# Optimization experiments

Measured on AMD Instinct MI355X. Metric: run time of the kernel, lower is better.

## Reference

```python
import jax, jax.numpy as jnp
import numpy as np

HIDDEN = 2048
HEAD_SIZE = 8
EXTRA = 4
NH = HEAD_SIZE * EXTRA          # 32 effective heads
D = HIDDEN // (HEAD_SIZE * 16)  # 16 per-head dim
PROJ = NH * D                   # 512
# NOTE: the torch module scales by att_size**-0.5 where att_size is the
# PRE-division value hidden//head_size//4 = 64, not the per-head dim D=16.
SCALE = (HIDDEN // HEAD_SIZE // EXTRA) ** -0.5


def _xavier(key, out_dim, in_dim):
    bound = float(np.sqrt(6.0 / (in_dim + out_dim)))
    return jax.random.uniform(key, (out_dim, in_dim), jnp.float32, -bound, bound)


def setup_inputs() -> dict:
    key = jax.random.key(0)
    ks = jax.random.split(key, 7)
    B, S = 2, 2048
    return {
        "q": jax.random.normal(ks[0], (B, S, HIDDEN), jnp.float32),
        "k": jax.random.normal(ks[1], (B, S, HIDDEN), jnp.float32),
        "v": jax.random.normal(ks[2], (B, S, HIDDEN), jnp.float32),
        "Wq": _xavier(ks[3], PROJ, HIDDEN),
        "Wk": _xavier(ks[4], PROJ, HIDDEN),
        "Wv": _xavier(ks[5], PROJ, HIDDEN),
        "Wo": _xavier(ks[6], HIDDEN, PROJ),
    }


def reference(q, k, v, Wq, Wk, Wv, Wo):
    B, S, _ = q.shape
    # projections (torch Linear: x @ W.T), reshape to [B,S,heads,d]
    qh = (q @ Wq.T).reshape(B, S, NH, D)
    kh = (k @ Wk.T).reshape(B, S, NH, D)
    vh = (v @ Wv.T).reshape(B, S, NH, D)
    scores = jnp.einsum("bshd,bthd->bhst", qh * SCALE, kh)  # [B,NH,S,S]
    attn = jax.nn.softmax(scores, axis=-1)
    out = jnp.einsum("bhst,bthd->bshd", attn, vh).reshape(B, S, PROJ)
    return out @ Wo.T  # [B,S,HIDDEN]
```

## Files before the change

### kernel.cpp

```cpp
#include <hip/hip_runtime.h>

#define HIDDEN 2048
#define NH 32
#define HD 16
#define PROJ 512
#define SEQ 2048

using f32x4    = __attribute__((ext_vector_type(4))) float;
using bf16x8   = __attribute__((ext_vector_type(8))) __bf16;

__device__ __forceinline__ unsigned short f2bf(float x) {
  unsigned int u = __float_as_uint(x);
  u += 0x7FFFu + ((u >> 16) & 1u);
  return (unsigned short)(u >> 16);
}

__device__ __forceinline__ f32x4 mfma_bf16(bf16x8 a, bf16x8 b, f32x4 c) {
  return __builtin_amdgcn_mfma_f32_16x16x32_bf16(a, b, c, 0, 0, 0);
}

#define GLDS16(gptr, lptr)                                              \
  __builtin_amdgcn_global_load_lds(                                     \
      (const __attribute__((address_space(1))) unsigned int*)(gptr),    \
      (__attribute__((address_space(3))) unsigned int*)(lptr), 16, 0, 0)

__global__ __launch_bounds__(256)
void convw_kernel(const float* __restrict__ Wq, const float* __restrict__ Wk,
                  const float* __restrict__ Wv, const float* __restrict__ Wo,
                  unsigned short* __restrict__ Wqb, unsigned short* __restrict__ Wkb,
                  unsigned short* __restrict__ Wvb, unsigned short* __restrict__ Wob) {
  const int z = blockIdx.y;
  const float* src = (z == 0) ? Wq : (z == 1) ? Wk : (z == 2) ? Wv : Wo;
  unsigned short* dst = (z == 0) ? Wqb : (z == 1) ? Wkb : (z == 2) ? Wvb : Wob;
  const size_t i = ((size_t)blockIdx.x * 256 + threadIdx.x) * 4;
  f32x4 v = *(const f32x4*)(src + i);
  uint2 p;
  p.x = f2bf(v[0]) | ((unsigned)f2bf(v[1]) << 16);
  p.y = f2bf(v[2]) | ((unsigned)f2bf(v[3]) << 16);
  *(uint2*)(dst + i) = p;
}

__global__ __launch_bounds__(256)
void convx_kernel(const float* __restrict__ q, const float* __restrict__ k,
                  const float* __restrict__ v,
                  unsigned short* __restrict__ qb, unsigned short* __restrict__ kb,
                  unsigned short* __restrict__ vb) {
  const int z = blockIdx.y;
  const float* src = (z == 0) ? q : (z == 1) ? k : v;
  unsigned short* dst = (z == 0) ? qb : (z == 1) ? kb : vb;
  const size_t i = ((size_t)blockIdx.x * 256 + threadIdx.x) * 4;
  f32x4 x = *(const f32x4*)(src + i);
  uint2 p;
  p.x = f2bf(x[0]) | ((unsigned)f2bf(x[1]) << 16);
  p.y = f2bf(x[2]) | ((unsigned)f2bf(x[3]) << 16);
  *(uint2*)(dst + i) = p;
}

__global__ __launch_bounds__(256)
void proj_kernel(const unsigned short* __restrict__ qb,
                 const unsigned short* __restrict__ kb,
                 const unsigned short* __restrict__ vb,
                 const unsigned short* __restrict__ Wqb,
                 const unsigned short* __restrict__ Wkb,
                 const unsigned short* __restrict__ Wvb,
                 unsigned short* __restrict__ qh, unsigned short* __restrict__ kh,
                 unsigned short* __restrict__ vt) {
  const int lin = blockIdx.x;
  const int e = lin & 7;
  const int t = lin >> 3;
  const int colt = t & 3;
  const int j = t >> 2;
  const int y = e + 8 * j;
  const int z = y >> 6;
  const int row0 = (y & 63) * 64;
  const int col0 = colt * 128;

  const unsigned short* A = (z == 0) ? qb : (z == 1) ? kb : vb;
  const unsigned short* Wb = (z == 0) ? Wqb : (z == 1) ? Wkb : Wvb;
  const float scale = (z == 0) ? 0.18033688011112042f  : 1.0f;

  __shared__ unsigned short As[64 * 32];
  __shared__ unsigned short Bs[128 * 32];

  const int tid = threadIdx.x;
  const int w = tid >> 6;
  const int lane = tid & 63;
  const int ln = lane & 15;
  const int qd = lane >> 4;
  const int wm = w >> 1, wn = w & 1;

  const int aM = tid >> 2;
  const int aG = (tid & 3) ^ (aM & 3);
  int bN[2], bG[2];
#pragma unroll
  for (int s = 0; s < 2; s++) {
    int L = s * 256 + tid;
    bN[s] = L >> 2;
    bG[s] = (L & 3) ^ (bN[s] & 3);
  }

  f32x4 acc[2][4];
#pragma unroll
  for (int mi = 0; mi < 2; mi++)
#pragma unroll
    for (int ni = 0; ni < 4; ni++) acc[mi][ni] = (f32x4){0.f, 0.f, 0.f, 0.f};

  for (int k0 = 0; k0 < HIDDEN; k0 += 32) {
    GLDS16(A + (size_t)(row0 + aM) * HIDDEN + k0 + aG * 8, &As[tid * 8]);
#pragma unroll
    for (int s = 0; s < 2; s++)
      GLDS16(Wb + (size_t)(col0 + bN[s]) * HIDDEN + k0 + bG[s] * 8,
             &Bs[(s * 256 + tid) * 8]);
    __syncthreads();

    bf16x8 af[2], bfv[4];
#pragma unroll
    for (int mi = 0; mi < 2; mi++) {
      int m = wm * 32 + mi * 16 + ln;
      af[mi] = *(const bf16x8*)&As[(m * 4 + (qd ^ (m & 3))) * 8];
    }
#pragma unroll
    for (int ni = 0; ni < 4; ni++) {
      int n = wn * 64 + ni * 16 + ln;
      bfv[ni] = *(const bf16x8*)&Bs[(n * 4 + (qd ^ (n & 3))) * 8];
    }
#pragma unroll
    for (int mi = 0; mi < 2; mi++)
#pragma unroll
      for (int ni = 0; ni < 4; ni++)
        acc[mi][ni] = mfma_bf16(af[mi], bfv[ni], acc[mi][ni]);
    __syncthreads();
  }

  if (z == 2) {
#pragma unroll
    for (int mi = 0; mi < 2; mi++)
#pragma unroll
      for (int ni = 0; ni < 4; ni++) {
        int h = (col0 + wn * 64 + ni * 16) >> 4;
        int grow0 = row0 + wm * 32 + mi * 16 + qd * 4;
        int b = grow0 >> 11, s0 = grow0 & 2047;
        uint2 o2;
        o2.x = f2bf(acc[mi][ni][0]) | ((unsigned)f2bf(acc[mi][ni][1]) << 16);
        o2.y = f2bf(acc[mi][ni][2]) | ((unsigned)f2bf(acc[mi][ni][3]) << 16);
        *(uint2*)&vt[((size_t)(b * NH + h) * HD + ln) * SEQ + s0] = o2;
      }
  } else {
    unsigned short* out = (z == 0) ? qh : kh;
#pragma unroll
    for (int mi = 0; mi < 2; mi++)
#pragma unroll
      for (int ni = 0; ni < 4; ni++) {
        int h = (col0 + wn * 64 + ni * 16) >> 4;
#pragma unroll
        for (int r = 0; r < 4; r++) {
          int grow = row0 + wm * 32 + mi * 16 + qd * 4 + r;
          int b = grow >> 11, s = grow & 2047;
          out[((size_t)(b * NH + h) * SEQ + s) * HD + ln] = f2bf(acc[mi][ni][r] * scale);
        }
      }
  }
}

__global__ __launch_bounds__(256, 4)
void flash_kernel(const unsigned short* __restrict__ qh,
                  const unsigned short* __restrict__ kh,
                  const unsigned short* __restrict__ vt,
                  unsigned short* __restrict__ attnb) {
  const int bh = blockIdx.x;
  const int b = bh >> 5, h = bh & 31;
  const int q0 = blockIdx.y * 128;
  const size_t hoff = (size_t)bh * SEQ * HD;
  const unsigned short* Qp = qh + hoff;
  const unsigned short* Kp = kh + hoff;
  const unsigned short* Vth = vt + hoff;

  __shared__ unsigned short Qs[128 * 16];
  __shared__ unsigned short Ks[2][128 * 16];
  __shared__ unsigned short Vts[2][256 * 8];
  __shared__ unsigned short Ps[4][32 * 40];
  __shared__ __align__(16) unsigned short Zz[8];

  const int tid = threadIdx.x;
  const int w = tid >> 6;
  const int lane = tid & 63;
  const int ln = lane & 15;
  const int qd = lane >> 4;
  const bool hiq = (qd >= 2);

  if (tid < 8) Zz[tid] = 0;

  const int vD = tid >> 4;
  const int vG = (tid & 15) ^ vD;

  GLDS16(Qp + (size_t)q0 * HD + tid * 8, &Qs[tid * 8]);
  GLDS16(Kp + tid * 8, &Ks[0][tid * 8]);
  GLDS16(Vth + (size_t)vD * SEQ + vG * 8, &Vts[0][tid * 8]);
  __syncthreads();

  bf16x8 aq[2];
#pragma unroll
  for (int ni = 0; ni < 2; ni++) {
    const unsigned short* src =
        hiq ? Zz : &Qs[(w * 32 + ni * 16 + ln) * 16 + (qd & 1) * 8];
    aq[ni] = *(const bf16x8*)src;
  }

  float lsum[2] = {0.f, 0.f};
  f32x4 o_acc[2] = {{0.f, 0.f, 0.f, 0.f}, {0.f, 0.f, 0.f, 0.f}};
  unsigned short* Pw = &Ps[w][0];

  for (int t = 0; t < 16; t++) {
    const int buf = t & 1;
    if (t < 15) {
      GLDS16(Kp + (size_t)(t + 1) * 2048 + tid * 8, &Ks[buf ^ 1][tid * 8]);
      GLDS16(Vth + (size_t)vD * SEQ + (t + 1) * 128 + vG * 8, &Vts[buf ^ 1][tid * 8]);
    }
    const unsigned short* Kb = &Ks[buf][0];
    const unsigned short* Vb = &Vts[buf][0];

#pragma unroll
    for (int c = 0; c < 4; c++) {
      f32x4 sc[2][2];
#pragma unroll
      for (int hf = 0; hf < 2; hf++) {
        int tile = c * 2 + hf;
        const unsigned short* asrc =
            hiq ? Zz : &Kb[(tile * 16 + ln) * 16 + (qd & 1) * 8];
        bf16x8 ak = *(const bf16x8*)asrc;
#pragma unroll
        for (int ni = 0; ni < 2; ni++)
          sc[ni][hf] = mfma_bf16(ak, aq[ni], (f32x4){0.f, 0.f, 0.f, 0.f});
      }
      bf16x8 av = *(const bf16x8*)&Vb[(ln * 16 + ((c * 4 + qd) ^ ln)) * 8];

#pragma unroll
      for (int ni = 0; ni < 2; ni++) {
        float e0 = __builtin_amdgcn_exp2f(sc[ni][0][0]);
        float e1 = __builtin_amdgcn_exp2f(sc[ni][0][1]);
        float e2 = __builtin_amdgcn_exp2f(sc[ni][0][2]);
        float e3 = __builtin_amdgcn_exp2f(sc[ni][0][3]);
        float e4 = __builtin_amdgcn_exp2f(sc[ni][1][0]);
        float e5 = __builtin_amdgcn_exp2f(sc[ni][1][1]);
        float e6 = __builtin_amdgcn_exp2f(sc[ni][1][2]);
        float e7 = __builtin_amdgcn_exp2f(sc[ni][1][3]);
        lsum[ni] += ((e0 + e1) + (e2 + e3)) + ((e4 + e5) + (e6 + e7));
        unsigned int u0 = __float_as_uint(e0) + 0x8000u;
        unsigned int u1 = __float_as_uint(e1) + 0x8000u;
        unsigned int u2 = __float_as_uint(e2) + 0x8000u;
        unsigned int u3 = __float_as_uint(e3) + 0x8000u;
        unsigned int u4 = __float_as_uint(e4) + 0x8000u;
        unsigned int u5 = __float_as_uint(e5) + 0x8000u;
        unsigned int u6 = __float_as_uint(e6) + 0x8000u;
        unsigned int u7 = __float_as_uint(e7) + 0x8000u;
        unsigned int d0 = __builtin_amdgcn_perm(u1, u0, 0x07060302u);
        unsigned int d1 = __builtin_amdgcn_perm(u3, u2, 0x07060302u);
        unsigned int d2 = __builtin_amdgcn_perm(u5, u4, 0x07060302u);
        unsigned int d3 = __builtin_amdgcn_perm(u7, u6, 0x07060302u);
        *(uint2*)&Pw[(ni * 16 + ln) * 40 + qd * 4] = make_uint2(d0, d1);
        *(uint2*)&Pw[(ni * 16 + ln) * 40 + 16 + qd * 4] = make_uint2(d2, d3);
      }

#pragma unroll
      for (int ni = 0; ni < 2; ni++) {
        bf16x8 bp = *(const bf16x8*)&Pw[(ni * 16 + ln) * 40 + qd * 8];
        o_acc[ni] = mfma_bf16(av, bp, o_acc[ni]);
      }
    }
    __syncthreads();
  }

#pragma unroll
  for (int ni = 0; ni < 2; ni++) {
    float l = lsum[ni];
    l += __shfl_xor(l, 16, 64);
    l += __shfl_xor(l, 32, 64);
    float invl = 1.0f / l;
    int s = q0 + w * 32 + ni * 16 + ln;
    f32x4 res = o_acc[ni] * invl;
    uint2 o2;
    o2.x = f2bf(res[0]) | ((unsigned)f2bf(res[1]) << 16);
    o2.y = f2bf(res[2]) | ((unsigned)f2bf(res[3]) << 16);
    *(uint2*)&attnb[((size_t)(b * SEQ + s)) * PROJ + h * HD + qd * 4] = o2;
  }
}

__global__ __launch_bounds__(256)
void out_kernel(const unsigned short* __restrict__ attnb,
                const unsigned short* __restrict__ Wob,
                float* __restrict__ out) {
  const int lin = blockIdx.x;
  const int e = lin & 7;
  const int t = lin >> 3;
  const int col0 = (e * 2 + (t & 1)) * 128;
  const int row0 = (t >> 1) * 64;

  __shared__ unsigned short As[64 * 32];
  __shared__ unsigned short Bs[128 * 32];

  const int tid = threadIdx.x;
  const int w = tid >> 6;
  const int lane = tid & 63;
  const int ln = lane & 15;
  const int qd = lane >> 4;
  const int wm = w >> 1, wn = w & 1;

  const int aM = tid >> 2;
  const int aG = (tid & 3) ^ (aM & 3);
  int bN[2], bG[2];
#pragma unroll
  for (int s = 0; s < 2; s++) {
    int L = s * 256 + tid;
    bN[s] = L >> 2;
    bG[s] = (L & 3) ^ (bN[s] & 3);
  }

  f32x4 acc[2][4];
#pragma unroll
  for (int mi = 0; mi < 2; mi++)
#pragma unroll
    for (int ni = 0; ni < 4; ni++) acc[mi][ni] = (f32x4){0.f, 0.f, 0.f, 0.f};

  for (int k0 = 0; k0 < PROJ; k0 += 32) {
    GLDS16(attnb + (size_t)(row0 + aM) * PROJ + k0 + aG * 8, &As[tid * 8]);
#pragma unroll
    for (int s = 0; s < 2; s++)
      GLDS16(Wob + (size_t)(col0 + bN[s]) * PROJ + k0 + bG[s] * 8,
             &Bs[(s * 256 + tid) * 8]);
    __syncthreads();

    bf16x8 af[2], bfv[4];
#pragma unroll
    for (int mi = 0; mi < 2; mi++) {
      int m = wm * 32 + mi * 16 + ln;
      af[mi] = *(const bf16x8*)&As[(m * 4 + (qd ^ (m & 3))) * 8];
    }
#pragma unroll
    for (int ni = 0; ni < 4; ni++) {
      int n = wn * 64 + ni * 16 + ln;
      bfv[ni] = *(const bf16x8*)&Bs[(n * 4 + (qd ^ (n & 3))) * 8];
    }
#pragma unroll
    for (int mi = 0; mi < 2; mi++)
#pragma unroll
      for (int ni = 0; ni < 4; ni++)
        acc[mi][ni] = mfma_bf16(af[mi], bfv[ni], acc[mi][ni]);
    __syncthreads();
  }

#pragma unroll
  for (int mi = 0; mi < 2; mi++)
#pragma unroll
    for (int ni = 0; ni < 4; ni++) {
      int gcol = col0 + wn * 64 + ni * 16 + ln;
#pragma unroll
      for (int r = 0; r < 4; r++) {
        int grow = row0 + wm * 32 + mi * 16 + qd * 4 + r;
        out[(size_t)grow * HIDDEN + gcol] = acc[mi][ni][r];
      }
    }
}

extern "C" void kernel_launch(void* const* d_in, const int* in_sizes, int n_in,
                              void* d_out, int out_size, void* d_ws, size_t ws_size,
                              hipStream_t stream) {
  const float* q  = (const float*)d_in[0];
  const float* k  = (const float*)d_in[1];
  const float* v  = (const float*)d_in[2];
  const float* Wq = (const float*)d_in[3];
  const float* Wk = (const float*)d_in[4];
  const float* Wv = (const float*)d_in[5];
  const float* Wo = (const float*)d_in[6];

  char* ws = (char*)d_ws;
  const size_t MB = 1024 * 1024;
  unsigned short* qh    = (unsigned short*)(ws);
  unsigned short* kh    = (unsigned short*)(ws + 4 * MB);
  unsigned short* vt    = (unsigned short*)(ws + 8 * MB);
  unsigned short* attnb = (unsigned short*)(ws + 12 * MB);
  unsigned short* Wqb   = (unsigned short*)(ws + 16 * MB);
  unsigned short* Wkb   = (unsigned short*)(ws + 18 * MB);
  unsigned short* Wvb   = (unsigned short*)(ws + 20 * MB);
  unsigned short* Wob   = (unsigned short*)(ws + 22 * MB);
  unsigned short* qb    = (unsigned short*)(ws + 24 * MB);
  unsigned short* kb    = (unsigned short*)(ws + 40 * MB);
  unsigned short* vb    = (unsigned short*)(ws + 56 * MB);

  convw_kernel<<<dim3(1024, 4), dim3(256), 0, stream>>>(Wq, Wk, Wv, Wo, Wqb, Wkb, Wvb, Wob);
  convx_kernel<<<dim3(8192, 3), dim3(256), 0, stream>>>(q, k, v, qb, kb, vb);
  proj_kernel<<<dim3(768), dim3(256), 0, stream>>>(qb, kb, vb, Wqb, Wkb, Wvb, qh, kh, vt);
  flash_kernel<<<dim3(64, 16), dim3(256), 0, stream>>>(qh, kh, vt, attnb);
  out_kernel<<<dim3(1024), dim3(256), 0, stream>>>(attnb, Wob, (float*)d_out);

  (void)in_sizes; (void)n_in; (void)out_size; (void)ws_size;
}
```

Before: 274.6 us.

## Merge conversion kernels, swizzle Q/K LDS, pack softmax ops, vectorize output stores

Merges the weight and activation fp32→bf16 conversion kernels into one launch, which saves a kernel launch. The Q/K tiles are loaded into LDS with an XOR swizzle so reads hit fewer bank conflicts. The softmax row-sum now uses packed v_pk_add_f32, and the probabilities are converted to bf16 with v_cvt_pk_bf16_f32 instead of manual integer rounding. The output GEMM swaps its MFMA operands so each lane holds four contiguous columns, which allows 16-byte vector stores instead of scalar strided stores. The hardware convert rounds to nearest-even, slightly unlike the old add-0x8000 rounding.

```diff
diff --git a/kernel.cpp b/kernel.cpp
--- a/kernel.cpp
+++ b/kernel.cpp
@@ -7,6 +7,7 @@
 #define SEQ 2048
 
 using f32x4    = __attribute__((ext_vector_type(4))) float;
+using f32x2    = __attribute__((ext_vector_type(2))) float;
 using bf16x8   = __attribute__((ext_vector_type(8))) __bf16;
 
 __device__ __forceinline__ unsigned short f2bf(float x) {
@@ -19,36 +20,50 @@
   return __builtin_amdgcn_mfma_f32_16x16x32_bf16(a, b, c, 0, 0, 0);
 }
 
+__device__ __forceinline__ f32x2 pk_add(f32x2 a, f32x2 b) {
+  f32x2 d;
+  asm("v_pk_add_f32 %0, %1, %2" : "=v"(d) : "v"(a), "v"(b));
+  return d;
+}
+
+__device__ __forceinline__ unsigned int cvt_pk_bf16(float lo, float hi) {
+  unsigned int d;
+  asm("v_cvt_pk_bf16_f32 %0, %1, %2" : "=v"(d) : "v"(lo), "v"(hi));
+  return d;
+}
+
 #define GLDS16(gptr, lptr)                                              \
   __builtin_amdgcn_global_load_lds(                                     \
       (const __attribute__((address_space(1))) unsigned int*)(gptr),    \
       (__attribute__((address_space(3))) unsigned int*)(lptr), 16, 0, 0)
 
 __global__ __launch_bounds__(256)
-void convw_kernel(const float* __restrict__ Wq, const float* __restrict__ Wk,
-                  const float* __restrict__ Wv, const float* __restrict__ Wo,
-                  unsigned short* __restrict__ Wqb, unsigned short* __restrict__ Wkb,
-                  unsigned short* __restrict__ Wvb, unsigned short* __restrict__ Wob) {
-  const int z = blockIdx.y;
-  const float* src = (z == 0) ? Wq : (z == 1) ? Wk : (z == 2) ? Wv : Wo;
-  unsigned short* dst = (z == 0) ? Wqb : (z == 1) ? Wkb : (z == 2) ? Wvb : Wob;
-  const size_t i = ((size_t)blockIdx.x * 256 + threadIdx.x) * 4;
-  f32x4 v = *(const f32x4*)(src + i);
-  uint2 p;
-  p.x = f2bf(v[0]) | ((unsigned)f2bf(v[1]) << 16);
-  p.y = f2bf(v[2]) | ((unsigned)f2bf(v[3]) << 16);
-  *(uint2*)(dst + i) = p;
-}
-
-__global__ __launch_bounds__(256)
-void convx_kernel(const float* __restrict__ q, const float* __restrict__ k,
-                  const float* __restrict__ v,
-                  unsigned short* __restrict__ qb, unsigned short* __restrict__ kb,
-                  unsigned short* __restrict__ vb) {
-  const int z = blockIdx.y;
-  const float* src = (z == 0) ? q : (z == 1) ? k : v;
-  unsigned short* dst = (z == 0) ? qb : (z == 1) ? kb : vb;
-  const size_t i = ((size_t)blockIdx.x * 256 + threadIdx.x) * 4;
+void conv_kernel(const float* __restrict__ q, const float* __restrict__ k,
+                 const float* __restrict__ v,
+                 const float* __restrict__ Wq, const float* __restrict__ Wk,
+                 const float* __restrict__ Wv, const float* __restrict__ Wo,
+                 unsigned short* __restrict__ qb, unsigned short* __restrict__ kb,
+                 unsigned short* __restrict__ vb,
+                 unsigned short* __restrict__ Wqb, unsigned short* __restrict__ Wkb,
+                 unsigned short* __restrict__ Wvb, unsigned short* __restrict__ Wob) {
+  const int bid = blockIdx.x;
+  const float* src;
+  unsigned short* dst;
+  size_t i;
+  if (bid < 24576) {
+    const int z = bid >> 13;
+    const int off = bid & 8191;
+    src = (z == 0) ? q : (z == 1) ? k : v;
+    dst = (z == 0) ? qb : (z == 1) ? kb : vb;
+    i = ((size_t)off * 256 + threadIdx.x) * 4;
+  } else {
+    const int r = bid - 24576;
+    const int z = r >> 10;
+    const int off = r & 1023;
+    src = (z == 0) ? Wq : (z == 1) ? Wk : (z == 2) ? Wv : Wo;
+    dst = (z == 0) ? Wqb : (z == 1) ? Wkb : (z == 2) ? Wvb : Wob;
+    i = ((size_t)off * 256 + threadIdx.x) * 4;
+  }
   f32x4 x = *(const f32x4*)(src + i);
   uint2 p;
   p.x = f2bf(x[0]) | ((unsigned)f2bf(x[1]) << 16);
@@ -193,8 +208,11 @@
   const int vD = tid >> 4;
   const int vG = (tid & 15) ^ vD;
 
-  GLDS16(Qp + (size_t)q0 * HD + tid * 8, &Qs[tid * 8]);
-  GLDS16(Kp + tid * 8, &Ks[0][tid * 8]);
+  const int qkOff = (tid >> 1) * 16 + (((tid & 1) ^ ((tid >> 3) & 1)) * 8);
+  const int hsel = ((qd & 1) ^ ((ln >> 2) & 1)) * 8;
+
+  GLDS16(Qp + (size_t)q0 * HD + qkOff, &Qs[tid * 8]);
+  GLDS16(Kp + qkOff, &Ks[0][tid * 8]);
   GLDS16(Vth + (size_t)vD * SEQ + vG * 8, &Vts[0][tid * 8]);
   __syncthreads();
 
@@ -202,18 +220,18 @@
 #pragma unroll
   for (int ni = 0; ni < 2; ni++) {
     const unsigned short* src =
-        hiq ? Zz : &Qs[(w * 32 + ni * 16 + ln) * 16 + (qd & 1) * 8];
+        hiq ? Zz : &Qs[(w * 32 + ni * 16 + ln) * 16 + hsel];
     aq[ni] = *(const bf16x8*)src;
   }
 
-  float lsum[2] = {0.f, 0.f};
+  f32x2 lsum2[2] = {{0.f, 0.f}, {0.f, 0.f}};
   f32x4 o_acc[2] = {{0.f, 0.f, 0.f, 0.f}, {0.f, 0.f, 0.f, 0.f}};
   unsigned short* Pw = &Ps[w][0];
 
   for (int t = 0; t < 16; t++) {
     const int buf = t & 1;
     if (t < 15) {
-      GLDS16(Kp + (size_t)(t + 1) * 2048 + tid * 8, &Ks[buf ^ 1][tid * 8]);
+      GLDS16(Kp + (size_t)(t + 1) * 2048 + qkOff, &Ks[buf ^ 1][tid * 8]);
       GLDS16(Vth + (size_t)vD * SEQ + (t + 1) * 128 + vG * 8, &Vts[buf ^ 1][tid * 8]);
     }
     const unsigned short* Kb = &Ks[buf][0];
@@ -226,7 +244,7 @@
       for (int hf = 0; hf < 2; hf++) {
         int tile = c * 2 + hf;
         const unsigned short* asrc =
-            hiq ? Zz : &Kb[(tile * 16 + ln) * 16 + (qd & 1) * 8];
+            hiq ? Zz : &Kb[(tile * 16 + ln) * 16 + hsel];
         bf16x8 ak = *(const bf16x8*)asrc;
 #pragma unroll
         for (int ni = 0; ni < 2; ni++)
@@ -244,19 +262,13 @@
         float e5 = __builtin_amdgcn_exp2f(sc[ni][1][1]);
         float e6 = __builtin_amdgcn_exp2f(sc[ni][1][2]);
         float e7 = __builtin_amdgcn_exp2f(sc[ni][1][3]);
-        lsum[ni] += ((e0 + e1) + (e2 + e3)) + ((e4 + e5) + (e6 + e7));
-        unsigned int u0 = __float_as_uint(e0) + 0x8000u;
-        unsigned int u1 = __float_as_uint(e1) + 0x8000u;
-        unsigned int u2 = __float_as_uint(e2) + 0x8000u;
-        unsigned int u3 = __float_as_uint(e3) + 0x8000u;
-        unsigned int u4 = __float_as_uint(e4) + 0x8000u;
-        unsigned int u5 = __float_as_uint(e5) + 0x8000u;
-        unsigned int u6 = __float_as_uint(e6) + 0x8000u;
-        unsigned int u7 = __float_as_uint(e7) + 0x8000u;
-        unsigned int d0 = __builtin_amdgcn_perm(u1, u0, 0x07060302u);
-        unsigned int d1 = __builtin_amdgcn_perm(u3, u2, 0x07060302u);
-        unsigned int d2 = __builtin_amdgcn_perm(u5, u4, 0x07060302u);
-        unsigned int d3 = __builtin_amdgcn_perm(u7, u6, 0x07060302u);
+        f32x2 s01 = pk_add((f32x2){e0, e1}, (f32x2){e2, e3});
+        f32x2 s23 = pk_add((f32x2){e4, e5}, (f32x2){e6, e7});
+        lsum2[ni] = pk_add(lsum2[ni], pk_add(s01, s23));
+        unsigned int d0 = cvt_pk_bf16(e0, e1);
+        unsigned int d1 = cvt_pk_bf16(e2, e3);
+        unsigned int d2 = cvt_pk_bf16(e4, e5);
+        unsigned int d3 = cvt_pk_bf16(e6, e7);
         *(uint2*)&Pw[(ni * 16 + ln) * 40 + qd * 4] = make_uint2(d0, d1);
         *(uint2*)&Pw[(ni * 16 + ln) * 40 + 16 + qd * 4] = make_uint2(d2, d3);
       }
@@ -272,7 +284,7 @@
 
 #pragma unroll
   for (int ni = 0; ni < 2; ni++) {
-    float l = lsum[ni];
+    float l = lsum2[ni][0] + lsum2[ni][1];
     l += __shfl_xor(l, 16, 64);
     l += __shfl_xor(l, 32, 64);
     float invl = 1.0f / l;
@@ -344,21 +356,19 @@
     for (int mi = 0; mi < 2; mi++)
 #pragma unroll
       for (int ni = 0; ni < 4; ni++)
-        acc[mi][ni] = mfma_bf16(af[mi], bfv[ni], acc[mi][ni]);
+        acc[mi][ni] = mfma_bf16(bfv[ni], af[mi], acc[mi][ni]);
     __syncthreads();
   }
 
 #pragma unroll
-  for (int mi = 0; mi < 2; mi++)
+  for (int mi = 0; mi < 2; mi++) {
+    int grow = row0 + wm * 32 + mi * 16 + ln;
 #pragma unroll
     for (int ni = 0; ni < 4; ni++) {
-      int gcol = col0 + wn * 64 + ni * 16 + ln;
-#pragma unroll
-      for (int r = 0; r < 4; r++) {
-        int grow = row0 + wm * 32 + mi * 16 + qd * 4 + r;
-        out[(size_t)grow * HIDDEN + gcol] = acc[mi][ni][r];
-      }
-    }
+      int gcol = col0 + wn * 64 + ni * 16 + qd * 4;
+      *(f32x4*)&out[(size_t)grow * HIDDEN + gcol] = acc[mi][ni];
+    }
+  }
 }
 
 extern "C" void kernel_launch(void* const* d_in, const int* in_sizes, int n_in,
@@ -386,8 +396,8 @@
   unsigned short* kb    = (unsigned short*)(ws + 40 * MB);
   unsigned short* vb    = (unsigned short*)(ws + 56 * MB);
 
-  convw_kernel<<<dim3(1024, 4), dim3(256), 0, stream>>>(Wq, Wk, Wv, Wo, Wqb, Wkb, Wvb, Wob);
-  convx_kernel<<<dim3(8192, 3), dim3(256), 0, stream>>>(q, k, v, qb, kb, vb);
+  conv_kernel<<<dim3(28672), dim3(256), 0, stream>>>(q, k, v, Wq, Wk, Wv, Wo,
+                                                     qb, kb, vb, Wqb, Wkb, Wvb, Wob);
   proj_kernel<<<dim3(768), dim3(256), 0, stream>>>(qb, kb, vb, Wqb, Wkb, Wvb, qh, kh, vt);
   flash_kernel<<<dim3(64, 16), dim3(256), 0, stream>>>(qh, kh, vt, attnb);
   out_kernel<<<dim3(1024), dim3(256), 0, stream>>>(attnb, Wob, (float*)d_out);
```

After: 266.6 us. 1.03x faster.
